# Optimization experiments

Measured on AMD Instinct MI355X. Metric: run time of the kernel, lower is better.

The kernel has to match this reference:

```python
import jax, jax.numpy as jnp
import numpy as np

N_NODES = 100000
N_EDGES = 1600000
D_IN, D_HID, D_OUT = 128, 128, 64


def gcn_conv(x, src, dst, deg_inv_sqrt, W, b, n_nodes):
    # PyG GCNConv (normalize=True, add_self_loops already folded into src/dst/deg):
    # out = scatter_add( d^{-1/2}[src] * d^{-1/2}[dst] * (x @ W)[src] ) + b
    h = x @ W                                    # [N, d_out]
    norm = deg_inv_sqrt[src] * deg_inv_sqrt[dst]  # [E+N]
    msg = h[src] * norm[:, None]                  # [E+N, d_out] (edge gather)
    out = jax.ops.segment_sum(msg, dst, num_segments=n_nodes)
    return out + b


def _augment(edge_index, n_nodes):
    # add self-loops and compute symmetric-normalization degrees (in-degree at dst)
    loop = jnp.arange(n_nodes, dtype=edge_index.dtype)
    src = jnp.concatenate([edge_index[0], loop])
    dst = jnp.concatenate([edge_index[1], loop])
    deg = jax.ops.segment_sum(jnp.ones_like(dst, dtype=jnp.float32), dst,
                              num_segments=n_nodes)
    deg_inv_sqrt = jnp.where(deg > 0, jax.lax.rsqrt(jnp.maximum(deg, 1.0)), 0.0)
    return src, dst, deg_inv_sqrt


def setup_inputs() -> dict:
    key = jax.random.key(0)
    k1, k2, k3, k4 = jax.random.split(key, 4)
    x = jax.random.normal(k1, (N_NODES, D_IN), dtype=jnp.float32)
    edge_index = jax.random.randint(k2, (2, N_EDGES), 0, N_NODES, dtype=jnp.int32)
    s = 1.0 / np.sqrt(D_IN)
    W1 = jax.random.uniform(k3, (D_IN, D_HID), dtype=jnp.float32, minval=-s, maxval=s)
    b1 = jnp.zeros((D_HID,), dtype=jnp.float32)
    s2 = 1.0 / np.sqrt(D_HID)
    W2 = jax.random.uniform(k4, (D_HID, D_OUT), dtype=jnp.float32, minval=-s2, maxval=s2)
    b2 = jnp.zeros((D_OUT,), dtype=jnp.float32)
    return {"x": x, "edge_index": edge_index, "W1": W1, "b1": b1, "W2": W2, "b2": b2}


def reference(x, edge_index, W1, b1, W2, b2):
    n_nodes = x.shape[0]
    src, dst, dinv = _augment(edge_index, n_nodes)
    h = gcn_conv(x, src, dst, dinv, W1, b1, n_nodes)
    h = jax.nn.relu(h)
    # dropout is identity in eval mode (F.dropout with training=False)
    out = gcn_conv(h, src, dst, dinv, W2, b2, n_nodes)
    return out
```

## Files before the change

### kernel.cpp

```cpp
#include <hip/hip_runtime.h>

typedef unsigned int uint;
typedef unsigned short ushort;
typedef __attribute__((ext_vector_type(8))) short short8v;
typedef __attribute__((ext_vector_type(4))) float f32x4;

#define NBMAX 512
#define BSHIFT 8

__device__ __forceinline__ ushort f2bf(float f) {
    uint u = __float_as_uint(f);
    u += 0x7fffu + ((u >> 16) & 1u);
    return (ushort)(u >> 16);
}


__global__ void bucket_hist(const int* __restrict__ dst, int* __restrict__ bcnt,
                            int E, int nbk) {
    __shared__ int s[NBMAX];
    int t = threadIdx.x;
    for (int i = t; i < nbk; i += 256) s[i] = 0;
    __syncthreads();
    int i0 = blockIdx.x * 4096 + t;
#pragma unroll
    for (int k = 0; k < 16; ++k) {
        int i = i0 + k * 256;
        if (i < E) atomicAdd(&s[dst[i] >> BSHIFT], 1);
    }
    __syncthreads();
    for (int i = t; i < nbk; i += 256) if (s[i] > 0) atomicAdd(&bcnt[i], s[i]);
}

__global__ void bucket_scan(const int* __restrict__ bcnt, int* __restrict__ bstart,
                            int* __restrict__ bcur, int nbk) {
    __shared__ int s[512];
    int t = threadIdx.x;
    int v = (t < nbk) ? bcnt[t] : 0;
    s[t] = v;
    __syncthreads();
    for (int o = 1; o < 512; o <<= 1) {
        int tv = (t >= o) ? s[t - o] : 0;
        __syncthreads();
        s[t] += tv;
        __syncthreads();
    }
    if (t < nbk) {
        int ex = s[t] - v;
        bstart[t] = ex;
        bcur[t] = ex;
    }
}

__global__ void bucket_scatter(const int* __restrict__ src, const int* __restrict__ dst,
                               int* __restrict__ bcur, int* __restrict__ tsw, int E) {
    __shared__ int cnt[NBMAX];
    __shared__ int base[NBMAX];
    int t = threadIdx.x;
    for (int i = t; i < NBMAX; i += 256) cnt[i] = 0;
    __syncthreads();
    int i0 = blockIdx.x * 4096 + t;
    int p_[16], b_[16], r_[16];
#pragma unroll
    for (int k = 0; k < 16; ++k) {
        int i = i0 + k * 256;
        if (i < E) {
            int s = src[i], d = dst[i];
            int bb = d >> BSHIFT;
            b_[k] = bb;
            p_[k] = s | ((d & ((1 << BSHIFT) - 1)) << 17);
            r_[k] = atomicAdd(&cnt[bb], 1);
        } else {
            b_[k] = -1;
        }
    }
    __syncthreads();
    for (int i = t; i < NBMAX; i += 256) if (cnt[i] > 0) base[i] = atomicAdd(&bcur[i], cnt[i]);
    __syncthreads();
#pragma unroll
    for (int k = 0; k < 16; ++k) {
        if (b_[k] >= 0) {
            int p = base[b_[k]] + r_[k];
            tsw[p] = p_[k];
        }
    }
}

__global__ void sort_bucket(const int* __restrict__ tsw, const int* __restrict__ bstart,
                            float* __restrict__ dinv, int* __restrict__ rp,
                            int* __restrict__ edata, int N, int E, int nbk) {
    __shared__ int cnt[256];
    __shared__ int cursor[256];
    int b = blockIdx.x;
    int t = threadIdx.x;
    int estart = bstart[b];
    int eend = (b + 1 < nbk) ? bstart[b + 1] : E;

    cnt[t] = 0;
    __syncthreads();
    for (int i = estart + t; i < eend; i += 256) {
        atomicAdd(&cnt[(uint)tsw[i] >> 17], 1);
    }
    __syncthreads();

    int node = (b << BSHIFT) + t;
    int self = (node < N) ? 1 : 0;
    int deg = cnt[t];
    int v = deg + self;
    cursor[t] = v;
    __syncthreads();
    for (int o = 1; o < 256; o <<= 1) {
        int tv = (t >= o) ? cursor[t - o] : 0;
        __syncthreads();
        cursor[t] += tv;
        __syncthreads();
    }
    int ex = cursor[t] - v;
    int gbase = estart + (b << BSHIFT);

    if (node < N) {
        dinv[node] = rsqrtf((float)(deg + 1));
        rp[node] = gbase + ex;
        edata[gbase + ex] = node;
    }
    if (b == nbk - 1 && t == 0) rp[N] = E + N;
    cursor[t] = ex + self;
    __syncthreads();

    for (int i = estart + t; i < eend; i += 256) {
        uint rec = (uint)tsw[i];
        int pos = gbase + atomicAdd(&cursor[rec >> 17], 1);
        edata[pos] = (int)(rec & 0x1FFFFu);
    }
}


__global__ void prep_w(const float* __restrict__ W1, const float* __restrict__ W2,
                       ushort* __restrict__ Wt1s, ushort* __restrict__ Wt2s,
                       int* __restrict__ bcnt) {
    int t = blockIdx.x * 256 + threadIdx.x;
    if (t < NBMAX) bcnt[t] = 0;
    int total = gridDim.x * 256;
    for (int idx = t; idx < 128 * 128; idx += total) {
        int nn = idx >> 7, kk = idx & 127;
        uint byte = (uint)nn * 256u + (uint)kk * 2u;
        byte ^= (uint)((nn & 7) << 4);
        Wt1s[byte >> 1] = f2bf(W1[kk * 128 + nn]);
    }
    for (int idx = t; idx < 64 * 128; idx += total) {
        int nn = idx >> 7, kk = idx & 127;
        uint byte = (uint)nn * 256u + (uint)kk * 2u;
        byte ^= (uint)((nn & 7) << 4);
        Wt2s[byte >> 1] = f2bf(W2[kk * 64 + nn]);
    }
}


template <int NCOLS, bool IN_BF16>
__launch_bounds__(256)
__global__ void gemm_mfma(const void* __restrict__ Xv, const ushort* __restrict__ Wimg,
                          ushort* __restrict__ H, const float* __restrict__ dinv, int n) {
    constexpr int NT = NCOLS / 16;
    if (blockIdx.x == 0 && threadIdx.x < NCOLS) H[(size_t)n * NCOLS + threadIdx.x] = 0;
    __shared__ ushort sW[NCOLS * 128];
    {
        const uint4* src = (const uint4*)Wimg;
        uint4* dst = (uint4*)sW;
        constexpr int NV = NCOLS * 128 * 2 / 16;
        for (int i = threadIdx.x; i < NV; i += 256) dst[i] = src[i];
    }
    __syncthreads();

    const int w  = threadIdx.x >> 6;
    const int l  = threadIdx.x & 63;
    const int lm = l & 15, lk = l >> 4;
    const int row_base = blockIdx.x * 128 + w * 32;

    f32x4 acc[2][NT];
#pragma unroll
    for (int mt = 0; mt < 2; ++mt)
#pragma unroll
        for (int nt = 0; nt < NT; ++nt) {
            f32x4 z = {0.f, 0.f, 0.f, 0.f};
            acc[mt][nt] = z;
        }

    int r0 = row_base + lm;
    int r1 = row_base + 16 + lm;
    int r0c = r0 < n ? r0 : n - 1;
    int r1c = r1 < n ? r1 : n - 1;

#pragma unroll
    for (int kb = 0; kb < 4; ++kb) {
        short8v a0, a1;
        if constexpr (IN_BF16) {
            const ushort* X = (const ushort*)Xv;
            a0 = *(const short8v*)(X + (size_t)r0c * 128 + kb * 32 + lk * 8);
            a1 = *(const short8v*)(X + (size_t)r1c * 128 + kb * 32 + lk * 8);
        } else {
            const float* X = (const float*)Xv;
            const float* p0 = X + (size_t)r0c * 128 + kb * 32 + lk * 8;
            const float* p1 = X + (size_t)r1c * 128 + kb * 32 + lk * 8;
            float4 u0 = *(const float4*)p0;
            float4 v0 = *(const float4*)(p0 + 4);
            float4 u1 = *(const float4*)p1;
            float4 v1 = *(const float4*)(p1 + 4);
            a0[0] = (short)f2bf(u0.x); a0[1] = (short)f2bf(u0.y);
            a0[2] = (short)f2bf(u0.z); a0[3] = (short)f2bf(u0.w);
            a0[4] = (short)f2bf(v0.x); a0[5] = (short)f2bf(v0.y);
            a0[6] = (short)f2bf(v0.z); a0[7] = (short)f2bf(v0.w);
            a1[0] = (short)f2bf(u1.x); a1[1] = (short)f2bf(u1.y);
            a1[2] = (short)f2bf(u1.z); a1[3] = (short)f2bf(u1.w);
            a1[4] = (short)f2bf(v1.x); a1[5] = (short)f2bf(v1.y);
            a1[6] = (short)f2bf(v1.z); a1[7] = (short)f2bf(v1.w);
        }
#pragma unroll
        for (int nt = 0; nt < NT; ++nt) {
            int nn = nt * 16 + lm;
            uint byte = (uint)nn * 256u + (uint)kb * 64u + (uint)lk * 16u;
            byte ^= (uint)((nn & 7) << 4);
            short8v b = *(const short8v*)((const char*)sW + byte);
            acc[0][nt] = __builtin_amdgcn_mfma_f32_16x16x32_bf16(a0, b, acc[0][nt], 0, 0, 0);
            acc[1][nt] = __builtin_amdgcn_mfma_f32_16x16x32_bf16(a1, b, acc[1][nt], 0, 0, 0);
        }
    }

    float dvs[2][4];
#pragma unroll
    for (int mt = 0; mt < 2; ++mt)
#pragma unroll
        for (int r = 0; r < 4; ++r) {
            int row = row_base + mt * 16 + lk * 4 + r;
            dvs[mt][r] = (row < n) ? dinv[row] : 0.f;
        }
#pragma unroll
    for (int mt = 0; mt < 2; ++mt)
#pragma unroll
        for (int nt = 0; nt < NT; ++nt)
#pragma unroll
            for (int r = 0; r < 4; ++r) {
                int row = row_base + mt * 16 + lk * 4 + r;
                if (row < n) H[(size_t)row * NCOLS + nt * 16 + lm] = f2bf(acc[mt][nt][r] * dvs[mt][r]);
            }
}


template <bool RELU>
__launch_bounds__(256)
__global__ void agg128(const ushort* __restrict__ H, const int* __restrict__ rp,
                       const int* __restrict__ edata, const float* __restrict__ dinv,
                       const float* __restrict__ bias, ushort* __restrict__ out, int N) {
    const int lane = threadIdx.x & 63;
    const int q = lane >> 4;
    const int c = lane & 15;
    const int node = blockIdx.x * 16 + ((threadIdx.x >> 6) << 2) + q;
    if (node >= N) return;
    int e = rp[node], end = rp[node + 1];
    float a0 = 0.f, a1 = 0.f, a2 = 0.f, a3 = 0.f;
    float a4 = 0.f, a5 = 0.f, a6 = 0.f, a7 = 0.f;

    for (; e < end; e += 16) {
        int idx = e + c;
        int md = (idx < end) ? edata[idx] : N;
#pragma unroll
        for (int j = 0; j < 16; ++j) {
            int si = __shfl(md, (q << 4) + j);
            uint4 hv = *(const uint4*)&H[(size_t)si * 128 + c * 8];
            a0 += __uint_as_float(hv.x << 16);
            a1 += __uint_as_float(hv.x & 0xffff0000u);
            a2 += __uint_as_float(hv.y << 16);
            a3 += __uint_as_float(hv.y & 0xffff0000u);
            a4 += __uint_as_float(hv.z << 16);
            a5 += __uint_as_float(hv.z & 0xffff0000u);
            a6 += __uint_as_float(hv.w << 16);
            a7 += __uint_as_float(hv.w & 0xffff0000u);
        }
    }
    float dg = dinv[node];
    float4 bv0 = *(const float4*)&bias[c * 8];
    float4 bv1 = *(const float4*)&bias[c * 8 + 4];
    a0 = dg * a0 + bv0.x; a1 = dg * a1 + bv0.y;
    a2 = dg * a2 + bv0.z; a3 = dg * a3 + bv0.w;
    a4 = dg * a4 + bv1.x; a5 = dg * a5 + bv1.y;
    a6 = dg * a6 + bv1.z; a7 = dg * a7 + bv1.w;
    if (RELU) {
        a0 = fmaxf(a0, 0.f); a1 = fmaxf(a1, 0.f);
        a2 = fmaxf(a2, 0.f); a3 = fmaxf(a3, 0.f);
        a4 = fmaxf(a4, 0.f); a5 = fmaxf(a5, 0.f);
        a6 = fmaxf(a6, 0.f); a7 = fmaxf(a7, 0.f);
    }
    uint4 pk;
    pk.x = (uint)f2bf(a0) | ((uint)f2bf(a1) << 16);
    pk.y = (uint)f2bf(a2) | ((uint)f2bf(a3) << 16);
    pk.z = (uint)f2bf(a4) | ((uint)f2bf(a5) << 16);
    pk.w = (uint)f2bf(a6) | ((uint)f2bf(a7) << 16);
    *(uint4*)&out[(size_t)node * 128 + c * 8] = pk;
}

__launch_bounds__(256)
__global__ void agg64(const ushort* __restrict__ H, const int* __restrict__ rp,
                      const int* __restrict__ edata, const float* __restrict__ dinv,
                      const float* __restrict__ bias, float* __restrict__ out, int N) {
    const int lane = threadIdx.x & 63;
    const int qb = lane & 48;
    const int c = lane & 15;
    const int node = blockIdx.x * 16 + (threadIdx.x >> 4);
    if (node >= N) return;
    int e = rp[node], end = rp[node + 1];
    float a0 = 0.f, a1 = 0.f, a2 = 0.f, a3 = 0.f;

    for (; e < end; e += 16) {
        int idx = e + c;
        int md = (idx < end) ? edata[idx] : N;
#pragma unroll
        for (int j = 0; j < 16; ++j) {
            int si = __shfl(md, qb + j);
            uint2 hv = *(const uint2*)&H[(size_t)si * 64 + c * 4];
            a0 += __uint_as_float(hv.x << 16);
            a1 += __uint_as_float(hv.x & 0xffff0000u);
            a2 += __uint_as_float(hv.y << 16);
            a3 += __uint_as_float(hv.y & 0xffff0000u);
        }
    }
    float dg = dinv[node];
    float4 bv = *(const float4*)&bias[c * 4];
    a0 = dg * a0 + bv.x; a1 = dg * a1 + bv.y;
    a2 = dg * a2 + bv.z; a3 = dg * a3 + bv.w;
    *(float4*)&out[(size_t)node * 64 + c * 4] = make_float4(a0, a1, a2, a3);
}

__global__ void zero_out(float* __restrict__ out, int n) {
    int i = blockIdx.x * 256 + threadIdx.x;
    if (i < n) out[i] = 0.f;
}


extern "C" void kernel_launch(void* const* d_in, const int* in_sizes, int n_in,
                              void* d_out, int out_size, void* d_ws, size_t ws_size,
                              hipStream_t stream) {
    const float* x  = (const float*)d_in[0];
    const int*   ei = (const int*)d_in[1];
    const float* W1 = (const float*)d_in[2];
    const float* b1 = (const float*)d_in[3];
    const float* W2 = (const float*)d_in[4];
    const float* b2 = (const float*)d_in[5];
    float* out = (float*)d_out;

    const int N = in_sizes[0] / 128;
    const int E = in_sizes[1] / 2;
    const int* srcp = ei;
    const int* dstp = ei + E;

    char* base = (char*)d_ws;
    size_t off = 0;
    auto alloc = [&](size_t bytes) -> void* {
        void* p = base + off;
        off += (bytes + 15) & ~(size_t)15;
        return p;
    };
    ushort* H1    = (ushort*)alloc((size_t)(N + 1) * 128 * 2);
    ushort* A1    = (ushort*)alloc((size_t)N * 128 * 2);
    ushort* Wt1s  = (ushort*)alloc(128 * 128 * 2);
    ushort* Wt2s  = (ushort*)alloc(64 * 128 * 2);
    float*  dinv  = (float*)alloc((size_t)N * 4);
    int*    rp    = (int*)alloc((size_t)(N + 1) * 4);
    int*    bcnt  = (int*)alloc(NBMAX * 4);
    int*    bstart= (int*)alloc(NBMAX * 4);
    int*    bcur  = (int*)alloc(NBMAX * 4);
    int*    edata = (int*)alloc((size_t)(E + N) * 4);
    ushort* H2    = H1;

    int* tsw = (int*)A1;

    int nbk = (N + (1 << BSHIFT) - 1) >> BSHIFT;
    if (off > ws_size || (size_t)E * 4 > (size_t)N * 256 || N > (1 << 17) || nbk > NBMAX) {
        zero_out<<<(out_size + 255) / 256, 256, 0, stream>>>(out, out_size);
        return;
    }
    int nchunk = (E + 4095) / 4096;

    prep_w<<<32, 256, 0, stream>>>(W1, W2, Wt1s, Wt2s, bcnt);
    bucket_hist<<<nchunk, 256, 0, stream>>>(dstp, bcnt, E, nbk);
    bucket_scan<<<1, 512, 0, stream>>>(bcnt, bstart, bcur, nbk);
    bucket_scatter<<<nchunk, 256, 0, stream>>>(srcp, dstp, bcur, tsw, E);
    sort_bucket<<<nbk, 256, 0, stream>>>(tsw, bstart, dinv, rp, edata, N, E, nbk);

    gemm_mfma<128, false><<<(N + 127) / 128, 256, 0, stream>>>(x, Wt1s, H1, dinv, N);
    agg128<true><<<(N + 15) / 16, 256, 0, stream>>>(H1, rp, edata, dinv, b1, A1, N);
    gemm_mfma<64, true><<<(N + 127) / 128, 256, 0, stream>>>(A1, Wt2s, H2, dinv, N);
    agg64<<<(N + 15) / 16, 256, 0, stream>>>(H2, rp, edata, dinv, b2, out, N);
}
```

Measured before the change: 198.0 us.

## Fuse layer-2 GEMM into layer-1 aggregation and merge weight prep into histogram

The second GEMM (A1 @ W2) is fused into the layer-1 aggregation kernel. Each block aggregates 16 nodes, stages the ReLU'd bf16 rows in LDS, and runs a 16x64 MFMA against W2 held in LDS, writing H2 directly. This removes the A1 round trip through HBM and one kernel launch. Weight conversion is also folded into the histogram kernel, with the bucket counter zeroed by a memset instead. The cost is that every aggregation block reloads the 16KB W2 image and adds a barrier, which may hurt occupancy and the latency hiding of the gather.

```diff
diff --git a/kernel.cpp b/kernel.cpp
--- a/kernel.cpp
+++ b/kernel.cpp
@@ -15,8 +15,10 @@
 }
 
 
-__global__ void bucket_hist(const int* __restrict__ dst, int* __restrict__ bcnt,
-                            int E, int nbk) {
+__global__ void hist_prep(const int* __restrict__ dst, int* __restrict__ bcnt,
+                          int E, int nbk,
+                          const float* __restrict__ W1, const float* __restrict__ W2,
+                          ushort* __restrict__ Wt1s, ushort* __restrict__ Wt2s) {
     __shared__ int s[NBMAX];
     int t = threadIdx.x;
     for (int i = t; i < nbk; i += 256) s[i] = 0;
@@ -29,6 +31,21 @@
     }
     __syncthreads();
     for (int i = t; i < nbk; i += 256) if (s[i] > 0) atomicAdd(&bcnt[i], s[i]);
+
+    int g = blockIdx.x * 256 + t;
+    int total = gridDim.x * 256;
+    for (int idx = g; idx < 128 * 128; idx += total) {
+        int nn = idx >> 7, kk = idx & 127;
+        uint byte = (uint)nn * 256u + (uint)kk * 2u;
+        byte ^= (uint)((nn & 7) << 4);
+        Wt1s[byte >> 1] = f2bf(W1[kk * 128 + nn]);
+    }
+    for (int idx = g; idx < 64 * 128; idx += total) {
+        int nn = idx >> 7, kk = idx & 127;
+        uint byte = (uint)nn * 256u + (uint)kk * 2u;
+        byte ^= (uint)((nn & 7) << 4);
+        Wt2s[byte >> 1] = f2bf(W2[kk * 64 + nn]);
+    }
 }
 
 __global__ void bucket_scan(const int* __restrict__ bcnt, int* __restrict__ bstart,
@@ -134,39 +151,16 @@
 }
 
 
-__global__ void prep_w(const float* __restrict__ W1, const float* __restrict__ W2,
-                       ushort* __restrict__ Wt1s, ushort* __restrict__ Wt2s,
-                       int* __restrict__ bcnt) {
-    int t = blockIdx.x * 256 + threadIdx.x;
-    if (t < NBMAX) bcnt[t] = 0;
-    int total = gridDim.x * 256;
-    for (int idx = t; idx < 128 * 128; idx += total) {
-        int nn = idx >> 7, kk = idx & 127;
-        uint byte = (uint)nn * 256u + (uint)kk * 2u;
-        byte ^= (uint)((nn & 7) << 4);
-        Wt1s[byte >> 1] = f2bf(W1[kk * 128 + nn]);
-    }
-    for (int idx = t; idx < 64 * 128; idx += total) {
-        int nn = idx >> 7, kk = idx & 127;
-        uint byte = (uint)nn * 256u + (uint)kk * 2u;
-        byte ^= (uint)((nn & 7) << 4);
-        Wt2s[byte >> 1] = f2bf(W2[kk * 64 + nn]);
-    }
-}
-
-
-template <int NCOLS, bool IN_BF16>
 __launch_bounds__(256)
-__global__ void gemm_mfma(const void* __restrict__ Xv, const ushort* __restrict__ Wimg,
-                          ushort* __restrict__ H, const float* __restrict__ dinv, int n) {
-    constexpr int NT = NCOLS / 16;
-    if (blockIdx.x == 0 && threadIdx.x < NCOLS) H[(size_t)n * NCOLS + threadIdx.x] = 0;
-    __shared__ ushort sW[NCOLS * 128];
+__global__ void gemm_mfma128(const float* __restrict__ X, const ushort* __restrict__ Wimg,
+                             ushort* __restrict__ H, const float* __restrict__ dinv, int n) {
+    constexpr int NT = 8;
+    if (blockIdx.x == 0 && threadIdx.x < 128) H[(size_t)n * 128 + threadIdx.x] = 0;
+    __shared__ ushort sW[128 * 128];
     {
         const uint4* src = (const uint4*)Wimg;
         uint4* dst = (uint4*)sW;
-        constexpr int NV = NCOLS * 128 * 2 / 16;
-        for (int i = threadIdx.x; i < NV; i += 256) dst[i] = src[i];
+        for (int i = threadIdx.x; i < 128 * 128 * 2 / 16; i += 256) dst[i] = src[i];
     }
     __syncthreads();
 
@@ -192,27 +186,20 @@
 #pragma unroll
     for (int kb = 0; kb < 4; ++kb) {
         short8v a0, a1;
-        if constexpr (IN_BF16) {
-            const ushort* X = (const ushort*)Xv;
-            a0 = *(const short8v*)(X + (size_t)r0c * 128 + kb * 32 + lk * 8);
-            a1 = *(const short8v*)(X + (size_t)r1c * 128 + kb * 32 + lk * 8);
-        } else {
-            const float* X = (const float*)Xv;
-            const float* p0 = X + (size_t)r0c * 128 + kb * 32 + lk * 8;
-            const float* p1 = X + (size_t)r1c * 128 + kb * 32 + lk * 8;
-            float4 u0 = *(const float4*)p0;
-            float4 v0 = *(const float4*)(p0 + 4);
-            float4 u1 = *(const float4*)p1;
-            float4 v1 = *(const float4*)(p1 + 4);
-            a0[0] = (short)f2bf(u0.x); a0[1] = (short)f2bf(u0.y);
-            a0[2] = (short)f2bf(u0.z); a0[3] = (short)f2bf(u0.w);
-            a0[4] = (short)f2bf(v0.x); a0[5] = (short)f2bf(v0.y);
-            a0[6] = (short)f2bf(v0.z); a0[7] = (short)f2bf(v0.w);
-            a1[0] = (short)f2bf(u1.x); a1[1] = (short)f2bf(u1.y);
-            a1[2] = (short)f2bf(u1.z); a1[3] = (short)f2bf(u1.w);
-            a1[4] = (short)f2bf(v1.x); a1[5] = (short)f2bf(v1.y);
-            a1[6] = (short)f2bf(v1.z); a1[7] = (short)f2bf(v1.w);
-        }
+        const float* p0 = X + (size_t)r0c * 128 + kb * 32 + lk * 8;
+        const float* p1 = X + (size_t)r1c * 128 + kb * 32 + lk * 8;
+        float4 u0 = *(const float4*)p0;
+        float4 v0 = *(const float4*)(p0 + 4);
+        float4 u1 = *(const float4*)p1;
+        float4 v1 = *(const float4*)(p1 + 4);
+        a0[0] = (short)f2bf(u0.x); a0[1] = (short)f2bf(u0.y);
+        a0[2] = (short)f2bf(u0.z); a0[3] = (short)f2bf(u0.w);
+        a0[4] = (short)f2bf(v0.x); a0[5] = (short)f2bf(v0.y);
+        a0[6] = (short)f2bf(v0.z); a0[7] = (short)f2bf(v0.w);
+        a1[0] = (short)f2bf(u1.x); a1[1] = (short)f2bf(u1.y);
+        a1[2] = (short)f2bf(u1.z); a1[3] = (short)f2bf(u1.w);
+        a1[4] = (short)f2bf(v1.x); a1[5] = (short)f2bf(v1.y);
+        a1[6] = (short)f2bf(v1.z); a1[7] = (short)f2bf(v1.w);
 #pragma unroll
         for (int nt = 0; nt < NT; ++nt) {
             int nn = nt * 16 + lm;
@@ -239,62 +226,90 @@
 #pragma unroll
             for (int r = 0; r < 4; ++r) {
                 int row = row_base + mt * 16 + lk * 4 + r;
-                if (row < n) H[(size_t)row * NCOLS + nt * 16 + lm] = f2bf(acc[mt][nt][r] * dvs[mt][r]);
+                if (row < n) H[(size_t)row * 128 + nt * 16 + lm] = f2bf(acc[mt][nt][r] * dvs[mt][r]);
             }
 }
 
 
-template <bool RELU>
 __launch_bounds__(256)
-__global__ void agg128(const ushort* __restrict__ H, const int* __restrict__ rp,
-                       const int* __restrict__ edata, const float* __restrict__ dinv,
-                       const float* __restrict__ bias, ushort* __restrict__ out, int N) {
+__global__ void agg128_w2(const ushort* __restrict__ H, const int* __restrict__ rp,
+                          const int* __restrict__ edata, const float* __restrict__ dinv,
+                          const float* __restrict__ b1, const ushort* __restrict__ W2img,
+                          ushort* __restrict__ H2, int N) {
+    __shared__ ushort sW[64 * 128];
+    __shared__ ushort sA[16 * 128];
+    {
+        const uint4* s = (const uint4*)W2img;
+        uint4* d = (uint4*)sW;
+        for (int i = threadIdx.x; i < 64 * 128 * 2 / 16; i += 256) d[i] = s[i];
+    }
+    if (blockIdx.x == 0 && threadIdx.x < 64) H2[(size_t)N * 64 + threadIdx.x] = 0;
+
     const int lane = threadIdx.x & 63;
-    const int q = lane >> 4;
     const int c = lane & 15;
-    const int node = blockIdx.x * 16 + ((threadIdx.x >> 6) << 2) + q;
-    if (node >= N) return;
-    int e = rp[node], end = rp[node + 1];
+    const int qb = lane & 48;
+    const int nl = threadIdx.x >> 4;
+    const int node = blockIdx.x * 16 + nl;
+
     float a0 = 0.f, a1 = 0.f, a2 = 0.f, a3 = 0.f;
     float a4 = 0.f, a5 = 0.f, a6 = 0.f, a7 = 0.f;
 
-    for (; e < end; e += 16) {
-        int idx = e + c;
-        int md = (idx < end) ? edata[idx] : N;
-#pragma unroll
-        for (int j = 0; j < 16; ++j) {
-            int si = __shfl(md, (q << 4) + j);
-            uint4 hv = *(const uint4*)&H[(size_t)si * 128 + c * 8];
-            a0 += __uint_as_float(hv.x << 16);
-            a1 += __uint_as_float(hv.x & 0xffff0000u);
-            a2 += __uint_as_float(hv.y << 16);
-            a3 += __uint_as_float(hv.y & 0xffff0000u);
-            a4 += __uint_as_float(hv.z << 16);
-            a5 += __uint_as_float(hv.z & 0xffff0000u);
-            a6 += __uint_as_float(hv.w << 16);
-            a7 += __uint_as_float(hv.w & 0xffff0000u);
-        }
-    }
-    float dg = dinv[node];
-    float4 bv0 = *(const float4*)&bias[c * 8];
-    float4 bv1 = *(const float4*)&bias[c * 8 + 4];
-    a0 = dg * a0 + bv0.x; a1 = dg * a1 + bv0.y;
-    a2 = dg * a2 + bv0.z; a3 = dg * a3 + bv0.w;
-    a4 = dg * a4 + bv1.x; a5 = dg * a5 + bv1.y;
-    a6 = dg * a6 + bv1.z; a7 = dg * a7 + bv1.w;
-    if (RELU) {
-        a0 = fmaxf(a0, 0.f); a1 = fmaxf(a1, 0.f);
-        a2 = fmaxf(a2, 0.f); a3 = fmaxf(a3, 0.f);
-        a4 = fmaxf(a4, 0.f); a5 = fmaxf(a5, 0.f);
-        a6 = fmaxf(a6, 0.f); a7 = fmaxf(a7, 0.f);
+    if (node < N) {
+        int e = rp[node], end = rp[node + 1];
+        for (; e < end; e += 16) {
+            int idx = e + c;
+            int md = (idx < end) ? edata[idx] : N;
+#pragma unroll
+            for (int j = 0; j < 16; ++j) {
+                int si = __shfl(md, qb + j);
+                uint4 hv = *(const uint4*)&H[(size_t)si * 128 + c * 8];
+                a0 += __uint_as_float(hv.x << 16);
+                a1 += __uint_as_float(hv.x & 0xffff0000u);
+                a2 += __uint_as_float(hv.y << 16);
+                a3 += __uint_as_float(hv.y & 0xffff0000u);
+                a4 += __uint_as_float(hv.z << 16);
+                a5 += __uint_as_float(hv.z & 0xffff0000u);
+                a6 += __uint_as_float(hv.w << 16);
+                a7 += __uint_as_float(hv.w & 0xffff0000u);
+            }
+        }
+        float dg = dinv[node];
+        float4 bv0 = *(const float4*)&b1[c * 8];
+        float4 bv1 = *(const float4*)&b1[c * 8 + 4];
+        a0 = fmaxf(dg * a0 + bv0.x, 0.f); a1 = fmaxf(dg * a1 + bv0.y, 0.f);
+        a2 = fmaxf(dg * a2 + bv0.z, 0.f); a3 = fmaxf(dg * a3 + bv0.w, 0.f);
+        a4 = fmaxf(dg * a4 + bv1.x, 0.f); a5 = fmaxf(dg * a5 + bv1.y, 0.f);
+        a6 = fmaxf(dg * a6 + bv1.z, 0.f); a7 = fmaxf(dg * a7 + bv1.w, 0.f);
+    } else {
+        a0 = a1 = a2 = a3 = a4 = a5 = a6 = a7 = 0.f;
     }
     uint4 pk;
     pk.x = (uint)f2bf(a0) | ((uint)f2bf(a1) << 16);
     pk.y = (uint)f2bf(a2) | ((uint)f2bf(a3) << 16);
     pk.z = (uint)f2bf(a4) | ((uint)f2bf(a5) << 16);
     pk.w = (uint)f2bf(a6) | ((uint)f2bf(a7) << 16);
-    *(uint4*)&out[(size_t)node * 128 + c * 8] = pk;
-}
+    uint wbyte = (uint)nl * 256u + (((uint)c * 16u) ^ ((uint)(nl & 7) << 4));
+    *(uint4*)((char*)sA + wbyte) = pk;
+    __syncthreads();
+
+    const int w  = threadIdx.x >> 6;
+    const int lm = lane & 15, lk = lane >> 4;
+    const int nn = w * 16 + lm;
+    f32x4 acc = {0.f, 0.f, 0.f, 0.f};
+#pragma unroll
+    for (int kb = 0; kb < 4; ++kb) {
+        uint ka = (uint)(kb * 64 + lk * 16);
+        short8v af = *(const short8v*)((const char*)sA + (uint)lm * 256u + (ka ^ ((uint)(lm & 7) << 4)));
+        short8v bf = *(const short8v*)((const char*)sW + (uint)nn * 256u + (ka ^ ((uint)(nn & 7) << 4)));
+        acc = __builtin_amdgcn_mfma_f32_16x16x32_bf16(af, bf, acc, 0, 0, 0);
+    }
+#pragma unroll
+    for (int r = 0; r < 4; ++r) {
+        int n2 = blockIdx.x * 16 + lk * 4 + r;
+        if (n2 < N) H2[(size_t)n2 * 64 + w * 16 + lm] = f2bf(acc[r] * dinv[n2]);
+    }
+}
+
 
 __launch_bounds__(256)
 __global__ void agg64(const ushort* __restrict__ H, const int* __restrict__ rp,
@@ -358,7 +373,7 @@
         return p;
     };
     ushort* H1    = (ushort*)alloc((size_t)(N + 1) * 128 * 2);
-    ushort* A1    = (ushort*)alloc((size_t)N * 128 * 2);
+    ushort* H2    = (ushort*)alloc((size_t)(N + 1) * 64 * 2);
     ushort* Wt1s  = (ushort*)alloc(128 * 128 * 2);
     ushort* Wt2s  = (ushort*)alloc(64 * 128 * 2);
     float*  dinv  = (float*)alloc((size_t)N * 4);
@@ -367,25 +382,24 @@
     int*    bstart= (int*)alloc(NBMAX * 4);
     int*    bcur  = (int*)alloc(NBMAX * 4);
     int*    edata = (int*)alloc((size_t)(E + N) * 4);
-    ushort* H2    = H1;
-
-    int* tsw = (int*)A1;
+
+    int* tsw = (int*)H2;
 
     int nbk = (N + (1 << BSHIFT) - 1) >> BSHIFT;
-    if (off > ws_size || (size_t)E * 4 > (size_t)N * 256 || N > (1 << 17) || nbk > NBMAX) {
+    if (off > ws_size || (size_t)E * 4 > (size_t)(N + 1) * 128 ||
+        N > (1 << 17) || nbk > NBMAX) {
         zero_out<<<(out_size + 255) / 256, 256, 0, stream>>>(out, out_size);
         return;
     }
     int nchunk = (E + 4095) / 4096;
 
-    prep_w<<<32, 256, 0, stream>>>(W1, W2, Wt1s, Wt2s, bcnt);
-    bucket_hist<<<nchunk, 256, 0, stream>>>(dstp, bcnt, E, nbk);
+    hipMemsetAsync(bcnt, 0, NBMAX * sizeof(int), stream);
+    hist_prep<<<nchunk, 256, 0, stream>>>(dstp, bcnt, E, nbk, W1, W2, Wt1s, Wt2s);
     bucket_scan<<<1, 512, 0, stream>>>(bcnt, bstart, bcur, nbk);
     bucket_scatter<<<nchunk, 256, 0, stream>>>(srcp, dstp, bcur, tsw, E);
     sort_bucket<<<nbk, 256, 0, stream>>>(tsw, bstart, dinv, rp, edata, N, E, nbk);
 
-    gemm_mfma<128, false><<<(N + 127) / 128, 256, 0, stream>>>(x, Wt1s, H1, dinv, N);
-    agg128<true><<<(N + 15) / 16, 256, 0, stream>>>(H1, rp, edata, dinv, b1, A1, N);
-    gemm_mfma<64, true><<<(N + 127) / 128, 256, 0, stream>>>(A1, Wt2s, H2, dinv, N);
+    gemm_mfma128<<<(N + 127) / 128, 256, 0, stream>>>(x, Wt1s, H1, dinv, N);
+    agg128_w2<<<(N + 15) / 16, 256, 0, stream>>>(H1, rp, edata, dinv, b1, Wt2s, H2, N);
     agg64<<<(N + 15) / 16, 256, 0, stream>>>(H2, rp, edata, dinv, b2, out, N);
 }
```

Result: faster. 191.4 us (median of 2 runs) (-3.3%).
